# Performance work log

Measured on AMD Instinct MI355X. Metric: run time of the kernel, lower is better.

Reference implementation:

```python
import jax, jax.numpy as jnp
import numpy as np

B = 2; S_LEN = 2048; D = 2048; E = 8; F = 5504
CAPACITY_FACTOR = 1.0; MIN_CAPACITY = 4; EPS = 1e-9


def setup_inputs() -> dict:
    key = jax.random.key(0)
    k1, k2, k3, k4, k5 = jax.random.split(key, 5)
    return {
        "hidden_states": jax.random.normal(k1, (B, S_LEN, D), jnp.float32),
        "wg": jax.random.normal(k2, (D, E), jnp.float32) * 0.02,
        "w1": jax.random.normal(k3, (E, D, F), jnp.float32) * 0.02,
        "w3": jax.random.normal(k4, (E, D, F), jnp.float32) * 0.02,
        "w2": jax.random.normal(k5, (E, F, D), jnp.float32) * 0.02,
    }


def _top2_gating(logits, capacity):
    # DeepSpeed-style top-2 gating with capacity-based token dropping.
    S, E_ = logits.shape
    gates = jax.nn.softmax(logits, axis=-1)                       # [S,E]
    idx1 = jnp.argmax(gates, axis=1)
    mask1 = jax.nn.one_hot(idx1, E_, dtype=gates.dtype)
    logits_no1 = jnp.where(mask1 > 0, -jnp.inf, logits)
    idx2 = jnp.argmax(logits_no1, axis=1)
    mask2 = jax.nn.one_hot(idx2, E_, dtype=gates.dtype)
    # load-balancing aux loss (computed before capacity drop)
    me = jnp.mean(gates, axis=0)
    ce = jnp.mean(mask1, axis=0)
    l_aux = jnp.mean(me * ce) * (E_ * E_)
    exp_counts = jnp.sum(mask1, axis=0).astype(jnp.int32)
    # position of each token within its expert's queue
    loc1 = jnp.cumsum(mask1, axis=0) - 1.0                        # [S,E]
    loc2 = jnp.cumsum(mask2, axis=0) - 1.0 + jnp.sum(mask1, axis=0, keepdims=True)
    mask1 = mask1 * (loc1 < capacity).astype(mask1.dtype)
    mask2 = mask2 * (loc2 < capacity).astype(mask2.dtype)
    loc1_s = jnp.sum(loc1 * mask1, axis=1).astype(jnp.int32)      # [S]
    loc2_s = jnp.sum(loc2 * mask2, axis=1).astype(jnp.int32)
    g1 = jnp.sum(gates * mask1, axis=1)
    g2 = jnp.sum(gates * mask2, axis=1)
    denom = jnp.clip(g1 + g2, EPS, None)
    g1 = g1 / denom
    g2 = g2 / denom
    oh1 = jax.nn.one_hot(loc1_s, capacity, dtype=gates.dtype)     # [S,C]
    oh2 = jax.nn.one_hot(loc2_s, capacity, dtype=gates.dtype)
    combine = (g1[:, None, None] * mask1[:, :, None] * oh1[:, None, :]
               + g2[:, None, None] * mask2[:, :, None] * oh2[:, None, :])  # [S,E,C]
    dispatch = (combine > 0).astype(gates.dtype)
    return l_aux, combine, dispatch, exp_counts


def reference(hidden_states, wg, w1, w3, w2):
    B_, L_, D_ = hidden_states.shape
    x = hidden_states.reshape(-1, D_)                             # [S,D]
    S = x.shape[0]
    capacity = max(int(2 * S / E * CAPACITY_FACTOR), MIN_CAPACITY)
    logits = x @ wg                                               # [S,E]
    l_aux, combine, dispatch, exp_counts = _top2_gating(logits, capacity)
    # dispatch: gather tokens into per-expert capacity slots
    xe = jnp.einsum("sec,sd->ecd", dispatch, x)                  # [E,C,D]
    # per-expert SwiGLU FeedForward (grouped GEMMs)
    h = jax.nn.silu(jnp.einsum("ecd,edf->ecf", xe, w1)) * jnp.einsum("ecd,edf->ecf", xe, w3)
    eo = jnp.einsum("ecf,efd->ecd", h, w2)                       # [E,C,D]
    out = jnp.einsum("sec,ecd->sd", combine, eo).reshape(B_, L_, D_)
    return out, l_aux, exp_counts
```

## Files before the change

### kernel.cpp

```cpp
#include <hip/hip_runtime.h>
#include <hip/hip_bf16.h>


#define S_TOT 4096
#define DD 2048
#define EE 8
#define FF 5504
#define CAP 1024
#define OUT_MAIN (S_TOT * DD)

#define BM 128
#define BN 128
#define BK 32
#define BKP 40

typedef __bf16 bf16x8 __attribute__((ext_vector_type(8)));
typedef float f32x4 __attribute__((ext_vector_type(4)));

__device__ __forceinline__ unsigned short f2bf(float f) {
    unsigned int u = __builtin_bit_cast(unsigned int, f);
    unsigned int lsb = (u >> 16) & 1u;
    u += 0x7fffu + lsb;
    return (unsigned short)(u >> 16);
}

__global__ void k_logits(const float* __restrict__ x, const float* __restrict__ wg,
                         float* __restrict__ logits) {
    const int s = blockIdx.x;
    const int t = threadIdx.x;
    const float* xr = x + (size_t)s * DD;
    float part[EE];
#pragma unroll
    for (int e = 0; e < EE; ++e) part[e] = 0.f;
#pragma unroll
    for (int i = 0; i < DD / 256; ++i) {
        int d = t + i * 256;
        float xv = xr[d];
#pragma unroll
        for (int e = 0; e < EE; ++e) part[e] += xv * wg[d * EE + e];
    }
    __shared__ float red[256 * EE];
#pragma unroll
    for (int e = 0; e < EE; ++e) red[t * EE + e] = part[e];
    __syncthreads();
    for (int off = 128; off > 0; off >>= 1) {
        if (t < off) {
#pragma unroll
            for (int e = 0; e < EE; ++e) red[t * EE + e] += red[(t + off) * EE + e];
        }
        __syncthreads();
    }
    if (t < EE) logits[(size_t)s * EE + t] = red[t];
}

__global__ void k_gating(const float* __restrict__ logits,
                         int* __restrict__ slot1, float* __restrict__ gw1,
                         int* __restrict__ slot2, float* __restrict__ gw2,
                         float* __restrict__ out_extra) {
    const int t = threadIdx.x;
    __shared__ int c1[256][EE];
    __shared__ int c2[256][EE];
    __shared__ float mesh[256][EE];
    __shared__ int tot1[EE];
    __shared__ float me_tot[EE];

    int i1[16], i2[16];
    float g1[16], g2[16];
    int lc1[EE], lc2[EE];
    float lme[EE];
#pragma unroll
    for (int e = 0; e < EE; ++e) { lc1[e] = 0; lc2[e] = 0; lme[e] = 0.f; }

    for (int k = 0; k < 16; ++k) {
        int s = t * 16 + k;
        float lg[EE];
        float m = -1e30f;
#pragma unroll
        for (int e = 0; e < EE; ++e) { lg[e] = logits[(size_t)s * EE + e]; m = fmaxf(m, lg[e]); }
        float ex[EE];
        float sum = 0.f;
#pragma unroll
        for (int e = 0; e < EE; ++e) { ex[e] = expf(lg[e] - m); sum += ex[e]; }
        float inv = 1.f / sum;
        float b1v = -1.f; int b1 = 0;
#pragma unroll
        for (int e = 0; e < EE; ++e) {
            float g = ex[e] * inv;
            lme[e] += g;
            if (g > b1v) { b1v = g; b1 = e; }
        }
        float b2l = -3.4e38f; int b2 = 0;
#pragma unroll
        for (int e = 0; e < EE; ++e) {
            if (e != b1 && lg[e] > b2l) { b2l = lg[e]; b2 = e; }
        }
        float b2v = ex[b2] * inv;
        i1[k] = b1; i2[k] = b2; g1[k] = b1v; g2[k] = b2v;
        lc1[b1]++; lc2[b2]++;
    }
#pragma unroll
    for (int e = 0; e < EE; ++e) { c1[t][e] = lc1[e]; c2[t][e] = lc2[e]; mesh[t][e] = lme[e]; }
    __syncthreads();
    if (t < 8) {
        int run = 0;
        for (int u = 0; u < 256; ++u) { int v = c1[u][t]; c1[u][t] = run; run += v; }
        tot1[t] = run;
    } else if (t < 16) {
        int e = t - 8; int run = 0;
        for (int u = 0; u < 256; ++u) { int v = c2[u][e]; c2[u][e] = run; run += v; }
    } else if (t < 24) {
        int e = t - 16; float sm = 0.f;
        for (int u = 0; u < 256; ++u) sm += mesh[u][e];
        me_tot[e] = sm;
    }
    __syncthreads();
    if (t == 0) {
        float la = 0.f;
        for (int e = 0; e < EE; ++e)
            la += (me_tot[e] / (float)S_TOT) * ((float)tot1[e] / (float)S_TOT);
        la *= (float)EE;
        out_extra[0] = la;
        for (int e = 0; e < EE; ++e) out_extra[1 + e] = (float)tot1[e];
    }
    int o1[EE], o2[EE];
#pragma unroll
    for (int e = 0; e < EE; ++e) { o1[e] = c1[t][e]; o2[e] = c2[t][e]; }
    for (int k = 0; k < 16; ++k) {
        int s = t * 16 + k;
        int e1 = i1[k]; int p1 = o1[e1]++;
        int e2 = i2[k]; int p2 = o2[e2]++ + tot1[e2];
        bool k1 = p1 < CAP, k2 = p2 < CAP;
        float a = k1 ? g1[k] : 0.f;
        float b = k2 ? g2[k] : 0.f;
        float den = fmaxf(a + b, 1e-9f);
        slot1[s] = k1 ? (e1 * CAP + p1) : -1;
        slot2[s] = k2 ? (e2 * CAP + p2) : -1;
        gw1[s] = a / den;
        gw2[s] = b / den;
    }
}

__global__ void k_zero(uint4* __restrict__ p, int n16) {
    int i = blockIdx.x * blockDim.x + threadIdx.x;
    if (i < n16) { uint4 z; z.x = 0; z.y = 0; z.z = 0; z.w = 0; p[i] = z; }
}

__global__ void k_scatter(const float* __restrict__ x, const int* __restrict__ slot1,
                          const int* __restrict__ slot2, unsigned short* __restrict__ xe) {
    const int s = blockIdx.x >> 1;
    const int sl = (blockIdx.x & 1) ? slot2[s] : slot1[s];
    if (sl < 0) return;
    const float* src = x + (size_t)s * DD;
    unsigned short* dst = xe + (size_t)sl * DD;
    const int d = threadIdx.x * 8;
    float4 u0 = *(const float4*)(src + d);
    float4 u1 = *(const float4*)(src + d + 4);
    union { unsigned short u[8]; uint4 v; } pk;
    pk.u[0] = f2bf(u0.x); pk.u[1] = f2bf(u0.y); pk.u[2] = f2bf(u0.z); pk.u[3] = f2bf(u0.w);
    pk.u[4] = f2bf(u1.x); pk.u[5] = f2bf(u1.y); pk.u[6] = f2bf(u1.z); pk.u[7] = f2bf(u1.w);
    *(uint4*)(dst + d) = pk.v;
}

__global__ __launch_bounds__(256, 2) void k_gemm1(const unsigned short* __restrict__ xe,
                                                  const float* __restrict__ w1,
                                                  const float* __restrict__ w3,
                                                  unsigned short* __restrict__ h) {
    const int e = blockIdx.z;
    const int cb = blockIdx.y * BM;
    const int fb = blockIdx.x * BN;
    const unsigned short* A = xe + (size_t)e * CAP * DD;
    const float* W1 = w1 + (size_t)e * DD * FF;
    const float* W3 = w3 + (size_t)e * DD * FF;
    __shared__ unsigned short As[BM * BK];
    __shared__ unsigned short B1s[BN * BKP];
    __shared__ unsigned short B3s[BN * BKP];
    const int t = threadIdx.x;
    const int wave = t >> 6, lane = t & 63;
    const int wm = (wave >> 1) * 64, wn = (wave & 1) * 64;
    const int lrow = lane & 15, quad = lane >> 4;
    f32x4 acc1[4][4], acc3[4][4];
#pragma unroll
    for (int i = 0; i < 4; ++i)
#pragma unroll
        for (int j = 0; j < 4; ++j) {
            acc1[i][j] = (f32x4){0.f, 0.f, 0.f, 0.f};
            acc3[i][j] = (f32x4){0.f, 0.f, 0.f, 0.f};
        }
    const int kk = t >> 3;
    const int ffo = (t & 7) * 16;
    for (int k0 = 0; k0 < DD; k0 += BK) {
#pragma unroll
        for (int i = 0; i < 2; ++i) {
            int idx = t + i * 256;
            int r = idx >> 2, seg = idx & 3;
            *(uint4*)&As[r * BK + seg * 8] =
                *(const uint4*)&A[(size_t)(cb + r) * DD + k0 + seg * 8];
        }
        {
            const float* p1 = &W1[(size_t)(k0 + kk) * FF + fb + ffo];
            const float* p3 = &W3[(size_t)(k0 + kk) * FF + fb + ffo];
            float4 va[4], vc[4];
#pragma unroll
            for (int q = 0; q < 4; ++q) { va[q] = *(const float4*)(p1 + q * 4); }
#pragma unroll
            for (int q = 0; q < 4; ++q) { vc[q] = *(const float4*)(p3 + q * 4); }
            unsigned short* q1 = &B1s[ffo * BKP + kk];
            unsigned short* q3 = &B3s[ffo * BKP + kk];
#pragma unroll
            for (int q = 0; q < 4; ++q) {
                q1[(q * 4 + 0) * BKP] = f2bf(va[q].x);
                q1[(q * 4 + 1) * BKP] = f2bf(va[q].y);
                q1[(q * 4 + 2) * BKP] = f2bf(va[q].z);
                q1[(q * 4 + 3) * BKP] = f2bf(va[q].w);
                q3[(q * 4 + 0) * BKP] = f2bf(vc[q].x);
                q3[(q * 4 + 1) * BKP] = f2bf(vc[q].y);
                q3[(q * 4 + 2) * BKP] = f2bf(vc[q].z);
                q3[(q * 4 + 3) * BKP] = f2bf(vc[q].w);
            }
        }
        __syncthreads();
        bf16x8 af[4], bf1[4], bf3[4];
#pragma unroll
        for (int i = 0; i < 4; ++i)
            af[i] = *(const bf16x8*)&As[(wm + i * 16 + lrow) * BK + quad * 8];
#pragma unroll
        for (int j = 0; j < 4; ++j) {
            bf1[j] = *(const bf16x8*)&B1s[(wn + j * 16 + lrow) * BKP + quad * 8];
            bf3[j] = *(const bf16x8*)&B3s[(wn + j * 16 + lrow) * BKP + quad * 8];
        }
#pragma unroll
        for (int i = 0; i < 4; ++i)
#pragma unroll
            for (int j = 0; j < 4; ++j) {
                acc1[i][j] = __builtin_amdgcn_mfma_f32_16x16x32_bf16(af[i], bf1[j], acc1[i][j], 0, 0, 0);
                acc3[i][j] = __builtin_amdgcn_mfma_f32_16x16x32_bf16(af[i], bf3[j], acc3[i][j], 0, 0, 0);
            }
        __syncthreads();
    }
    unsigned short* H = h + (size_t)e * CAP * FF;
#pragma unroll
    for (int i = 0; i < 4; ++i)
#pragma unroll
        for (int j = 0; j < 4; ++j)
#pragma unroll
            for (int r = 0; r < 4; ++r) {
                float v1 = acc1[i][j][r], v3 = acc3[i][j][r];
                float hv = (v1 / (1.f + __expf(-v1))) * v3;
                int row = cb + wm + i * 16 + quad * 4 + r;
                int col = fb + wn + j * 16 + lrow;
                H[(size_t)row * FF + col] = f2bf(hv);
            }
}

__global__ __launch_bounds__(256, 2) void k_gemm2(const unsigned short* __restrict__ h,
                                                  const float* __restrict__ w2,
                                                  float* __restrict__ eo) {
    const int e = blockIdx.z;
    const int cb = blockIdx.y * BM;
    const int db = blockIdx.x * BN;
    const unsigned short* A = h + (size_t)e * CAP * FF;
    const float* W = w2 + (size_t)e * FF * DD;
    __shared__ unsigned short As[BM * BK];
    __shared__ unsigned short Bs[BN * BKP];
    const int t = threadIdx.x;
    const int wave = t >> 6, lane = t & 63;
    const int wm = (wave >> 1) * 64, wn = (wave & 1) * 64;
    const int lrow = lane & 15, quad = lane >> 4;
    f32x4 acc[4][4];
#pragma unroll
    for (int i = 0; i < 4; ++i)
#pragma unroll
        for (int j = 0; j < 4; ++j) acc[i][j] = (f32x4){0.f, 0.f, 0.f, 0.f};
    const int kk = t >> 3;
    const int ffo = (t & 7) * 16;
    for (int k0 = 0; k0 < FF; k0 += BK) {
#pragma unroll
        for (int i = 0; i < 2; ++i) {
            int idx = t + i * 256;
            int r = idx >> 2, seg = idx & 3;
            *(uint4*)&As[r * BK + seg * 8] =
                *(const uint4*)&A[(size_t)(cb + r) * FF + k0 + seg * 8];
        }
        {
            const float* p = &W[(size_t)(k0 + kk) * DD + db + ffo];
            float4 v[4];
#pragma unroll
            for (int q = 0; q < 4; ++q) v[q] = *(const float4*)(p + q * 4);
            unsigned short* qb = &Bs[ffo * BKP + kk];
#pragma unroll
            for (int q = 0; q < 4; ++q) {
                qb[(q * 4 + 0) * BKP] = f2bf(v[q].x);
                qb[(q * 4 + 1) * BKP] = f2bf(v[q].y);
                qb[(q * 4 + 2) * BKP] = f2bf(v[q].z);
                qb[(q * 4 + 3) * BKP] = f2bf(v[q].w);
            }
        }
        __syncthreads();
        bf16x8 af[4], bf[4];
#pragma unroll
        for (int i = 0; i < 4; ++i)
            af[i] = *(const bf16x8*)&As[(wm + i * 16 + lrow) * BK + quad * 8];
#pragma unroll
        for (int j = 0; j < 4; ++j)
            bf[j] = *(const bf16x8*)&Bs[(wn + j * 16 + lrow) * BKP + quad * 8];
#pragma unroll
        for (int i = 0; i < 4; ++i)
#pragma unroll
            for (int j = 0; j < 4; ++j)
                acc[i][j] = __builtin_amdgcn_mfma_f32_16x16x32_bf16(af[i], bf[j], acc[i][j], 0, 0, 0);
        __syncthreads();
    }
    float* O = eo + (size_t)e * CAP * DD;
#pragma unroll
    for (int i = 0; i < 4; ++i)
#pragma unroll
        for (int j = 0; j < 4; ++j)
#pragma unroll
            for (int r = 0; r < 4; ++r) {
                int row = cb + wm + i * 16 + quad * 4 + r;
                int col = db + wn + j * 16 + lrow;
                O[(size_t)row * DD + col] = acc[i][j][r];
            }
}

__global__ void k_combine(const float* __restrict__ eo,
                          const int* __restrict__ slot1, const float* __restrict__ gw1,
                          const int* __restrict__ slot2, const float* __restrict__ gw2,
                          float* __restrict__ out) {
    const int s = blockIdx.x, t = threadIdx.x;
    const int sl1 = slot1[s], sl2 = slot2[s];
    const float a = gw1[s], b = gw2[s];
    const int d = t * 8;
    float r[8];
#pragma unroll
    for (int j = 0; j < 8; ++j) r[j] = 0.f;
    if (sl1 >= 0) {
        const float* p = eo + (size_t)sl1 * DD + d;
        float4 u0 = *(const float4*)p, u1 = *(const float4*)(p + 4);
        r[0] += a * u0.x; r[1] += a * u0.y; r[2] += a * u0.z; r[3] += a * u0.w;
        r[4] += a * u1.x; r[5] += a * u1.y; r[6] += a * u1.z; r[7] += a * u1.w;
    }
    if (sl2 >= 0) {
        const float* p = eo + (size_t)sl2 * DD + d;
        float4 u0 = *(const float4*)p, u1 = *(const float4*)(p + 4);
        r[0] += b * u0.x; r[1] += b * u0.y; r[2] += b * u0.z; r[3] += b * u0.w;
        r[4] += b * u1.x; r[5] += b * u1.y; r[6] += b * u1.z; r[7] += b * u1.w;
    }
    float* q = out + (size_t)s * DD + d;
    float4 w0, w1v;
    w0.x = r[0]; w0.y = r[1]; w0.z = r[2]; w0.w = r[3];
    w1v.x = r[4]; w1v.y = r[5]; w1v.z = r[6]; w1v.w = r[7];
    *(float4*)q = w0;
    *(float4*)(q + 4) = w1v;
}

extern "C" void kernel_launch(void* const* d_in, const int* in_sizes, int n_in,
                              void* d_out, int out_size, void* d_ws, size_t ws_size,
                              hipStream_t stream) {
    const float* x  = (const float*)d_in[0];
    const float* wg = (const float*)d_in[1];
    const float* w1 = (const float*)d_in[2];
    const float* w3 = (const float*)d_in[3];
    const float* w2 = (const float*)d_in[4];
    float* out = (float*)d_out;

    char* ws = (char*)d_ws;
    size_t off = 0;
    float* logits = (float*)(ws + off); off += (size_t)S_TOT * EE * 4;
    int* slot1    = (int*)(ws + off);   off += (size_t)S_TOT * 4;
    float* gw1    = (float*)(ws + off); off += (size_t)S_TOT * 4;
    int* slot2    = (int*)(ws + off);   off += (size_t)S_TOT * 4;
    float* gw2    = (float*)(ws + off); off += (size_t)S_TOT * 4;
    unsigned short* xe   = (unsigned short*)(ws + off); off += (size_t)EE * CAP * DD * 2;
    unsigned short* hbuf = (unsigned short*)(ws + off); off += (size_t)EE * CAP * FF * 2;
    float* eo     = (float*)(ws + off); off += (size_t)EE * CAP * DD * 4;

    k_logits<<<S_TOT, 256, 0, stream>>>(x, wg, logits);
    k_gating<<<1, 256, 0, stream>>>(logits, slot1, gw1, slot2, gw2, out + OUT_MAIN);
    int n16 = (int)((size_t)EE * CAP * DD * 2 / 16);
    k_zero<<<(n16 + 255) / 256, 256, 0, stream>>>((uint4*)xe, n16);
    k_scatter<<<S_TOT * 2, 256, 0, stream>>>(x, slot1, slot2, xe);
    k_gemm1<<<dim3(FF / BN, CAP / BM, EE), 256, 0, stream>>>(xe, w1, w3, hbuf);
    k_gemm2<<<dim3(DD / BN, CAP / BM, EE), 256, 0, stream>>>(hbuf, w2, eo);
    k_combine<<<S_TOT, 256, 0, stream>>>(eo, slot1, gw1, slot2, gw2, out);
}
```

Before: 2.356 ms.

## Pre-transpose expert weights to bf16 and use direct-to-LDS loads in GEMMs

```diff
diff --git a/kernel.cpp b/kernel.cpp
--- a/kernel.cpp
+++ b/kernel.cpp
@@ -1,5 +1,4 @@
 #include <hip/hip_runtime.h>
-#include <hip/hip_bf16.h>
 
 
 #define S_TOT 4096
@@ -16,12 +15,18 @@
 
 typedef __bf16 bf16x8 __attribute__((ext_vector_type(8)));
 typedef float f32x4 __attribute__((ext_vector_type(4)));
+typedef unsigned int u32;
 
 __device__ __forceinline__ unsigned short f2bf(float f) {
     unsigned int u = __builtin_bit_cast(unsigned int, f);
     unsigned int lsb = (u >> 16) & 1u;
     u += 0x7fffu + lsb;
     return (unsigned short)(u >> 16);
+}
+
+__device__ __forceinline__ void gload16(const void* g, void* l) {
+    __builtin_amdgcn_global_load_lds((const __attribute__((address_space(1))) u32*)g,
+                                     (__attribute__((address_space(3))) u32*)l, 16, 0, 0);
 }
 
 __global__ void k_logits(const float* __restrict__ x, const float* __restrict__ wg,
@@ -161,10 +166,186 @@
     *(uint4*)(dst + d) = pk.v;
 }
 
-__global__ __launch_bounds__(256, 2) void k_gemm1(const unsigned short* __restrict__ xe,
-                                                  const float* __restrict__ w1,
-                                                  const float* __restrict__ w3,
-                                                  unsigned short* __restrict__ h) {
+__global__ __launch_bounds__(256) void k_wtrans(const float* __restrict__ w1,
+                                                const float* __restrict__ w3,
+                                                const float* __restrict__ w2,
+                                                unsigned short* __restrict__ w1t,
+                                                unsigned short* __restrict__ w3t,
+                                                unsigned short* __restrict__ w2t,
+                                                int zbase) {
+    const int z = blockIdx.z + zbase;
+    const int m = z >> 3, e = z & 7;
+    const float* src;
+    unsigned short* dst;
+    int R, C, tx, ty;
+    if (m == 0) {
+        src = w1 + (size_t)e * DD * FF; dst = w1t + (size_t)e * FF * DD;
+        R = DD; C = FF; tx = blockIdx.x; ty = blockIdx.y;
+    } else if (m == 1) {
+        src = w3 + (size_t)e * DD * FF; dst = w3t + (size_t)e * FF * DD;
+        R = DD; C = FF; tx = blockIdx.x; ty = blockIdx.y;
+    } else {
+        src = w2 + (size_t)e * FF * DD; dst = w2t + (size_t)e * DD * FF;
+        R = FF; C = DD; tx = blockIdx.y; ty = blockIdx.x;
+    }
+    if (tx * 64 >= C || ty * 64 >= R) return;
+    const int r0 = ty * 64, c0 = tx * 64;
+    __shared__ u32 lds[64 * 35];
+    const int t = threadIdx.x;
+    const int sc = (t & 31) * 2;
+    const int srb = (t >> 5) * 2;
+#pragma unroll
+    for (int q = 0; q < 4; ++q) {
+        const int sr = srb + 16 * q;
+        const float* p = src + (size_t)(r0 + sr) * C + c0 + sc;
+        float2 a = *(const float2*)p;
+        float2 b = *(const float2*)(p + C);
+        lds[sc * 35 + (sr >> 1)]       = (u32)f2bf(a.x) | ((u32)f2bf(b.x) << 16);
+        lds[(sc + 1) * 35 + (sr >> 1)] = (u32)f2bf(a.y) | ((u32)f2bf(b.y) << 16);
+    }
+    __syncthreads();
+    const int cc = t >> 2, rq = (t & 3) * 4;
+    const u32* lp = &lds[cc * 35];
+    union { u32 w[4]; uint4 v; } o0, o1;
+#pragma unroll
+    for (int i = 0; i < 4; ++i) o0.w[i] = lp[rq + i];
+#pragma unroll
+    for (int i = 0; i < 4; ++i) o1.w[i] = lp[16 + rq + i];
+    unsigned short* dp = dst + (size_t)(c0 + cc) * R + r0;
+    *(uint4*)(dp + (t & 3) * 8) = o0.v;
+    *(uint4*)(dp + 32 + (t & 3) * 8) = o1.v;
+}
+
+__global__ __launch_bounds__(256, 2) void k_gemm1n(const unsigned short* __restrict__ xe,
+                                                   const unsigned short* __restrict__ w1t,
+                                                   const unsigned short* __restrict__ w3t,
+                                                   unsigned short* __restrict__ h) {
+    const int e = blockIdx.z;
+    const int cb = blockIdx.x * BM;
+    const int fb = blockIdx.y * BN;
+    __shared__ unsigned short As[BM * BK];
+    __shared__ unsigned short B1s[BN * BK];
+    __shared__ unsigned short B3s[BN * BK];
+    const int t = threadIdx.x;
+    const int wave = t >> 6, lane = t & 63;
+    const int wm = (wave >> 1) * 64, wn = (wave & 1) * 64;
+    const int lrow = lane & 15, quad = lane >> 4;
+    const int sr = wave * 16 + (lane >> 2);
+    const int sc = (lane & 3) * 8;
+    const unsigned short* pa  = xe  + (size_t)e * CAP * DD + (size_t)(cb + sr) * DD + sc;
+    const unsigned short* pb1 = w1t + (size_t)e * FF * DD + (size_t)(fb + sr) * DD + sc;
+    const unsigned short* pb3 = w3t + (size_t)e * FF * DD + (size_t)(fb + sr) * DD + sc;
+    const size_t row64 = (size_t)64 * DD;
+    f32x4 acc1[4][4], acc3[4][4];
+#pragma unroll
+    for (int i = 0; i < 4; ++i)
+#pragma unroll
+        for (int j = 0; j < 4; ++j) {
+            acc1[i][j] = (f32x4){0.f, 0.f, 0.f, 0.f};
+            acc3[i][j] = (f32x4){0.f, 0.f, 0.f, 0.f};
+        }
+    for (int k0 = 0; k0 < DD; k0 += BK) {
+        gload16(pa,          &As[wave * 512]);
+        gload16(pa + row64,  &As[2048 + wave * 512]);
+        gload16(pb1,         &B1s[wave * 512]);
+        gload16(pb1 + row64, &B1s[2048 + wave * 512]);
+        gload16(pb3,         &B3s[wave * 512]);
+        gload16(pb3 + row64, &B3s[2048 + wave * 512]);
+        pa += BK; pb1 += BK; pb3 += BK;
+        __syncthreads();
+        bf16x8 af[4], b1f[4], b3f[4];
+#pragma unroll
+        for (int i = 0; i < 4; ++i)
+            af[i] = *(const bf16x8*)&As[(wm + i * 16 + lrow) * BK + quad * 8];
+#pragma unroll
+        for (int j = 0; j < 4; ++j) {
+            b1f[j] = *(const bf16x8*)&B1s[(wn + j * 16 + lrow) * BK + quad * 8];
+            b3f[j] = *(const bf16x8*)&B3s[(wn + j * 16 + lrow) * BK + quad * 8];
+        }
+#pragma unroll
+        for (int i = 0; i < 4; ++i)
+#pragma unroll
+            for (int j = 0; j < 4; ++j) {
+                acc1[i][j] = __builtin_amdgcn_mfma_f32_16x16x32_bf16(af[i], b1f[j], acc1[i][j], 0, 0, 0);
+                acc3[i][j] = __builtin_amdgcn_mfma_f32_16x16x32_bf16(af[i], b3f[j], acc3[i][j], 0, 0, 0);
+            }
+        __syncthreads();
+    }
+    unsigned short* H = h + (size_t)e * CAP * FF;
+#pragma unroll
+    for (int i = 0; i < 4; ++i)
+#pragma unroll
+        for (int j = 0; j < 4; ++j)
+#pragma unroll
+            for (int r = 0; r < 4; ++r) {
+                float v1 = acc1[i][j][r], v3 = acc3[i][j][r];
+                float hv = (v1 / (1.f + __expf(-v1))) * v3;
+                int row = cb + wm + i * 16 + quad * 4 + r;
+                int col = fb + wn + j * 16 + lrow;
+                H[(size_t)row * FF + col] = f2bf(hv);
+            }
+}
+
+__global__ __launch_bounds__(256, 2) void k_gemm2n(const unsigned short* __restrict__ h,
+                                                   const unsigned short* __restrict__ w2t,
+                                                   float* __restrict__ eo) {
+    const int e = blockIdx.z;
+    const int cb = blockIdx.x * BM;
+    const int db = blockIdx.y * BN;
+    __shared__ unsigned short As[BM * BK];
+    __shared__ unsigned short Bs[BN * BK];
+    const int t = threadIdx.x;
+    const int wave = t >> 6, lane = t & 63;
+    const int wm = (wave >> 1) * 64, wn = (wave & 1) * 64;
+    const int lrow = lane & 15, quad = lane >> 4;
+    const int sr = wave * 16 + (lane >> 2);
+    const int sc = (lane & 3) * 8;
+    const unsigned short* pa = h   + (size_t)e * CAP * FF + (size_t)(cb + sr) * FF + sc;
+    const unsigned short* pb = w2t + (size_t)e * DD * FF + (size_t)(db + sr) * FF + sc;
+    const size_t row64 = (size_t)64 * FF;
+    f32x4 acc[4][4];
+#pragma unroll
+    for (int i = 0; i < 4; ++i)
+#pragma unroll
+        for (int j = 0; j < 4; ++j) acc[i][j] = (f32x4){0.f, 0.f, 0.f, 0.f};
+    for (int k0 = 0; k0 < FF; k0 += BK) {
+        gload16(pa,         &As[wave * 512]);
+        gload16(pa + row64, &As[2048 + wave * 512]);
+        gload16(pb,         &Bs[wave * 512]);
+        gload16(pb + row64, &Bs[2048 + wave * 512]);
+        pa += BK; pb += BK;
+        __syncthreads();
+        bf16x8 af[4], bf[4];
+#pragma unroll
+        for (int i = 0; i < 4; ++i)
+            af[i] = *(const bf16x8*)&As[(wm + i * 16 + lrow) * BK + quad * 8];
+#pragma unroll
+        for (int j = 0; j < 4; ++j)
+            bf[j] = *(const bf16x8*)&Bs[(wn + j * 16 + lrow) * BK + quad * 8];
+#pragma unroll
+        for (int i = 0; i < 4; ++i)
+#pragma unroll
+            for (int j = 0; j < 4; ++j)
+                acc[i][j] = __builtin_amdgcn_mfma_f32_16x16x32_bf16(af[i], bf[j], acc[i][j], 0, 0, 0);
+        __syncthreads();
+    }
+    float* O = eo + (size_t)e * CAP * DD;
+#pragma unroll
+    for (int i = 0; i < 4; ++i)
+#pragma unroll
+        for (int j = 0; j < 4; ++j)
+#pragma unroll
+            for (int r = 0; r < 4; ++r) {
+                int row = cb + wm + i * 16 + quad * 4 + r;
+                int col = db + wn + j * 16 + lrow;
+                O[(size_t)row * DD + col] = acc[i][j][r];
+            }
+}
+
+__global__ __launch_bounds__(256, 2) void k_gemm1_fb(const unsigned short* __restrict__ xe,
+                                                     const float* __restrict__ w1,
+                                                     const float* __restrict__ w3,
+                                                     unsigned short* __restrict__ h) {
     const int e = blockIdx.z;
     const int cb = blockIdx.y * BM;
     const int fb = blockIdx.x * BN;
@@ -252,9 +433,9 @@
             }
 }
 
-__global__ __launch_bounds__(256, 2) void k_gemm2(const unsigned short* __restrict__ h,
-                                                  const float* __restrict__ w2,
-                                                  float* __restrict__ eo) {
+__global__ __launch_bounds__(256, 2) void k_gemm2_fb(const unsigned short* __restrict__ h,
+                                                     const float* __restrict__ w2,
+                                                     float* __restrict__ eo) {
     const int e = blockIdx.z;
     const int cb = blockIdx.y * BM;
     const int db = blockIdx.x * BN;
@@ -373,14 +554,42 @@
     float* gw2    = (float*)(ws + off); off += (size_t)S_TOT * 4;
     unsigned short* xe   = (unsigned short*)(ws + off); off += (size_t)EE * CAP * DD * 2;
     unsigned short* hbuf = (unsigned short*)(ws + off); off += (size_t)EE * CAP * FF * 2;
-    float* eo     = (float*)(ws + off); off += (size_t)EE * CAP * DD * 4;
+    const size_t wmat = (size_t)EE * (size_t)DD * (size_t)FF * 2;
+    const size_t need_big = off + 3 * wmat;
+    unsigned short* w2t_big = (unsigned short*)(ws + off);
+    unsigned short* w1t_big = (unsigned short*)(ws + off + wmat);
+    unsigned short* w3t_big = (unsigned short*)(ws + off + 2 * wmat);
+    float* eo_big = (float*)w1t_big;
+    const size_t need_g1 = off + 2 * wmat;
+    unsigned short* w1t_g1 = (unsigned short*)(ws + off);
+    unsigned short* w3t_g1 = (unsigned short*)(ws + off + wmat);
+    float* eo_g1 = (float*)w1t_g1;
+    float* eo_fb = (float*)(ws + off);
+
+    const int tier = (ws_size >= need_big) ? 2 : (ws_size >= need_g1) ? 1 : 0;
+
+    if (tier == 2)
+        k_wtrans<<<dim3(86, 32, 24), 256, 0, stream>>>(w1, w3, w2, w1t_big, w3t_big, w2t_big, 0);
+    else if (tier == 1)
+        k_wtrans<<<dim3(86, 32, 16), 256, 0, stream>>>(w1, w3, w2, w1t_g1, w3t_g1, nullptr, 0);
 
     k_logits<<<S_TOT, 256, 0, stream>>>(x, wg, logits);
     k_gating<<<1, 256, 0, stream>>>(logits, slot1, gw1, slot2, gw2, out + OUT_MAIN);
     int n16 = (int)((size_t)EE * CAP * DD * 2 / 16);
     k_zero<<<(n16 + 255) / 256, 256, 0, stream>>>((uint4*)xe, n16);
     k_scatter<<<S_TOT * 2, 256, 0, stream>>>(x, slot1, slot2, xe);
-    k_gemm1<<<dim3(FF / BN, CAP / BM, EE), 256, 0, stream>>>(xe, w1, w3, hbuf);
-    k_gemm2<<<dim3(DD / BN, CAP / BM, EE), 256, 0, stream>>>(hbuf, w2, eo);
-    k_combine<<<S_TOT, 256, 0, stream>>>(eo, slot1, gw1, slot2, gw2, out);
-}
+
+    if (tier == 2) {
+        k_gemm1n<<<dim3(CAP / BM, FF / BN, EE), 256, 0, stream>>>(xe, w1t_big, w3t_big, hbuf);
+        k_gemm2n<<<dim3(CAP / BM, DD / BN, EE), 256, 0, stream>>>(hbuf, w2t_big, eo_big);
+        k_combine<<<S_TOT, 256, 0, stream>>>(eo_big, slot1, gw1, slot2, gw2, out);
+    } else if (tier == 1) {
+        k_gemm1n<<<dim3(CAP / BM, FF / BN, EE), 256, 0, stream>>>(xe, w1t_g1, w3t_g1, hbuf);
+        k_gemm2_fb<<<dim3(DD / BN, CAP / BM, EE), 256, 0, stream>>>(hbuf, w2, eo_g1);
+        k_combine<<<S_TOT, 256, 0, stream>>>(eo_g1, slot1, gw1, slot2, gw2, out);
+    } else {
+        k_gemm1_fb<<<dim3(FF / BN, CAP / BM, EE), 256, 0, stream>>>(xe, w1, w3, hbuf);
+        k_gemm2_fb<<<dim3(DD / BN, CAP / BM, EE), 256, 0, stream>>>(hbuf, w2, eo_fb);
+        k_combine<<<S_TOT, 256, 0, stream>>>(eo_fb, slot1, gw1, slot2, gw2, out);
+    }
+}
```

New measurement: 1.991 ms. 1.18x faster.
